# Optimization experiments

Hardware: AMD Instinct MI355X
Metric: run time of the kernel (lower is better)

Reference implementation:

```python
import jax, jax.numpy as jnp
import numpy as np

N_NODES = 50000
N_EDGES = 800000
HIDDEN = 64
NUM_FEATURES = 1
OUT_DIM = 2


def setup_inputs() -> dict:
    key = jax.random.key(0)
    k = jax.random.split(key, 6)
    x = jax.random.normal(k[0], (N_NODES, NUM_FEATURES), dtype=jnp.float32)
    edge_index = jax.random.randint(k[1], (2, N_EDGES), 0, N_NODES, dtype=jnp.int32)
    # GCNConv params (PyG default: glorot weight, zero bias; random here for testing)
    W1 = jax.random.normal(k[2], (NUM_FEATURES, HIDDEN), dtype=jnp.float32) * 0.5
    b1 = jax.random.normal(k[3], (HIDDEN,), dtype=jnp.float32) * 0.1
    W2 = jax.random.normal(k[4], (HIDDEN, OUT_DIM), dtype=jnp.float32) * 0.1
    b2 = jax.random.normal(k[5], (OUT_DIM,), dtype=jnp.float32) * 0.1
    return {"x": x, "edge_index": edge_index, "W1": W1, "b1": b1, "W2": W2, "b2": b2}


def _gcn_norm(edge_index, num_nodes):
    # PyG gcn_norm with add_self_loops=True, symmetric normalization
    row, col = edge_index[0], edge_index[1]
    loop = jnp.arange(num_nodes, dtype=row.dtype)
    row = jnp.concatenate([row, loop])
    col = jnp.concatenate([col, loop])
    ew = jnp.ones(row.shape[0], dtype=jnp.float32)
    deg = jax.ops.segment_sum(ew, col, num_segments=num_nodes)  # in-degree incl. self-loop
    dinv = jnp.where(deg > 0, jax.lax.rsqrt(deg), 0.0)
    norm = dinv[row] * dinv[col]  # [E+N]
    return row, col, norm


def _gcn_conv(x, row, col, norm, W, b, num_nodes):
    h = x @ W                                  # [N, out] transform first (out <= in here is fine)
    msg = h[row] * norm[:, None]               # gather + scale, [E+N, out]
    out = jax.ops.segment_sum(msg, col, num_segments=num_nodes)  # scatter-add at targets
    return out + b


def reference(x, edge_index, W1, b1, W2, b2):
    row, col, norm = _gcn_norm(edge_index, N_NODES)
    h = _gcn_conv(x, row, col, norm, W1, b1, N_NODES)
    h = jax.nn.relu(h)
    out = _gcn_conv(h, row, col, norm, W2, b2, N_NODES)
    return out
```

## Files before the change

kernel.cpp:

```cpp
#include <hip/hip_runtime.h>
#include <math.h>

#define N_NODES 50000
#define N_EDGES 800000
#define HIDDEN  64
#define MAXDEG  64
#define NPB     64
#define NCHUNK  256
#define CHUNK   (N_EDGES / NCHUNK)
#define NGROUP  (N_NODES / 4)


__global__ __launch_bounds__(256)
void k_hist(const int* __restrict__ col, unsigned* __restrict__ part) {
    __shared__ unsigned h[NGROUP];
    const int c = blockIdx.x;
    for (int i = threadIdx.x; i < NGROUP; i += 256) h[i] = 0u;
    __syncthreads();
    const int* cc = col + c * CHUNK;
    for (int i = threadIdx.x; i < CHUNK; i += 256) {
        int n = cc[i];
        atomicAdd(&h[n >> 2], 1u << ((n & 3) * 8));
    }
    __syncthreads();
    unsigned* dst = part + (size_t)c * NGROUP;
    for (int i = threadIdx.x; i < NGROUP; i += 256) dst[i] = h[i];
}

__global__ __launch_bounds__(256)
void k_scan(unsigned* __restrict__ part, const float* __restrict__ x,
            unsigned* __restrict__ cntPacked, float* __restrict__ g) {
    int i = blockIdx.x * 256 + threadIdx.x;
    if (i >= NGROUP) return;
    unsigned run = 0;
    for (int c0 = 0; c0 < NCHUNK; c0 += 8) {
        unsigned v[8];
#pragma unroll
        for (int k = 0; k < 8; ++k) v[k] = part[(size_t)(c0 + k) * NGROUP + i];
#pragma unroll
        for (int k = 0; k < 8; ++k) {
            part[(size_t)(c0 + k) * NGROUP + i] = run;
            run += v[k];
        }
    }
    cntPacked[i] = run;
    int n0 = i * 4;
#pragma unroll
    for (int b = 0; b < 4; ++b) {
        int deg = (int)((run >> (8 * b)) & 255u);
        int n = n0 + b;
        g[n] = rsqrtf((float)(min(deg, MAXDEG) + 1)) * x[n];
    }
}

__global__ __launch_bounds__(256)
void k_place(const int* __restrict__ row, const int* __restrict__ col,
             const unsigned char* __restrict__ baseBytes,
             unsigned short* __restrict__ ell) {
    __shared__ unsigned h[NGROUP];
    const int c = blockIdx.x;
    for (int i = threadIdx.x; i < NGROUP; i += 256) h[i] = 0u;
    __syncthreads();
    const int* cc = col + c * CHUNK;
    const int* rr = row + c * CHUNK;
    const unsigned char* gb = baseBytes + (size_t)c * (size_t)N_NODES;
    for (int i = threadIdx.x; i < CHUNK; i += 256) {
        int n = cc[i];
        int sh = (n & 3) * 8;
        unsigned old = atomicAdd(&h[n >> 2], 1u << sh);
        int j = (int)((old >> sh) & 255u) + (int)gb[n];
        if (j < MAXDEG) ell[(size_t)j * N_NODES + n] = (unsigned short)rr[i];
    }
}

__global__ __launch_bounds__(512)
void k_layer1(const unsigned short* __restrict__ ell, const unsigned* __restrict__ cntPacked,
              const float* __restrict__ g,
              const float* __restrict__ W1, const float* __restrict__ b1,
              const float* __restrict__ W2, float2* __restrict__ z) {
    __shared__ float red[8][NPB];
    const int w = threadIdx.x >> 6;
    const int l = threadIdx.x & 63;
    const int n = blockIdx.x * NPB + l;
    const bool valid = (n < N_NODES);
    int d = valid ? min((int)((cntPacked[n >> 2] >> ((n & 3) * 8)) & 255u), MAXDEG) : 0;
    float acc = 0.0f;
    for (int j = w; j < d; j += 8)
        acc += g[ell[(size_t)j * N_NODES + n]];
    red[w][l] = acc;
    __syncthreads();
    if (w == 0 && valid) {
        float a = red[0][l] + red[1][l] + red[2][l] + red[3][l]
                + red[4][l] + red[5][l] + red[6][l] + red[7][l];
        float di = rsqrtf((float)(d + 1));
        float sv = di * (a + g[n]);
        float y0 = 0.0f, y1 = 0.0f;
#pragma unroll
        for (int k = 0; k < HIDDEN; ++k) {
            float h = fmaxf(sv * W1[k] + b1[k], 0.0f);
            y0 += h * W2[2 * k];
            y1 += h * W2[2 * k + 1];
        }
        z[n] = make_float2(di * y0, di * y1);
    }
}

__global__ __launch_bounds__(512)
void k_layer2(const unsigned short* __restrict__ ell, const unsigned* __restrict__ cntPacked,
              const float2* __restrict__ z, const float* __restrict__ b2,
              float2* __restrict__ out) {
    __shared__ float2 red[8][NPB];
    const int w = threadIdx.x >> 6;
    const int l = threadIdx.x & 63;
    const int n = blockIdx.x * NPB + l;
    const bool valid = (n < N_NODES);
    int d = valid ? min((int)((cntPacked[n >> 2] >> ((n & 3) * 8)) & 255u), MAXDEG) : 0;
    float T0 = 0.0f, T1 = 0.0f;
    for (int j = w; j < d; j += 8) {
        float2 v = z[ell[(size_t)j * N_NODES + n]];
        T0 += v.x; T1 += v.y;
    }
    red[w][l] = make_float2(T0, T1);
    __syncthreads();
    if (w == 0 && valid) {
        float Tx = 0.0f, Ty = 0.0f;
#pragma unroll
        for (int k = 0; k < 8; ++k) { Tx += red[k][l].x; Ty += red[k][l].y; }
        float di = rsqrtf((float)(d + 1));
        float2 zn = z[n];
        out[n] = make_float2(di * (Tx + zn.x) + b2[0], di * (Ty + zn.y) + b2[1]);
    }
}


extern "C" void kernel_launch(void* const* d_in, const int* in_sizes, int n_in,
                              void* d_out, int out_size, void* d_ws, size_t ws_size,
                              hipStream_t stream) {
    const float* x  = (const float*)d_in[0];
    const int*   ei = (const int*)d_in[1];
    const float* W1 = (const float*)d_in[2];
    const float* b1 = (const float*)d_in[3];
    const float* W2 = (const float*)d_in[4];
    const float* b2 = (const float*)d_in[5];

    const int* row = ei;
    const int* col = ei + N_EDGES;

    unsigned* part      = (unsigned*)d_ws;
    unsigned* cntPacked = part + (size_t)NCHUNK * NGROUP;
    float*    g         = (float*)(cntPacked + NGROUP);
    float2*   z         = (float2*)(g + N_NODES);
    unsigned short* ell = (unsigned short*)(z + N_NODES);

    const int gS = (NGROUP + 255) / 256;
    const int gL = (N_NODES + NPB - 1) / NPB;

    k_hist  <<<NCHUNK, 256, 0, stream>>>(col, part);
    k_scan  <<<gS, 256, 0, stream>>>(part, x, cntPacked, g);
    k_place <<<NCHUNK, 256, 0, stream>>>(row, col, (const unsigned char*)part, ell);
    k_layer1<<<gL, 512, 0, stream>>>(ell, cntPacked, g, W1, b1, W2, z);
    k_layer2<<<gL, 512, 0, stream>>>(ell, cntPacked, z, b2, (float2*)d_out);
}
```

Baseline: 121.1 us.

## Replace ELL build with LDS-privatized scatter-add aggregation per node range

Drops the exclusive scan and the ELL placement kernel. Each layer's aggregation now scatters edge contributions into shared-memory float accumulators covering a node-range slice, writes per-chunk partial sums, and a follow-up kernel reduces them. The MAXDEG cap goes away, so the degree handling is exact. The cost is that every block rereads the full edge chunk for each node slice, large partial-sum buffers are written and reduced, and the shared-memory float atomics may contend.

```diff
diff --git a/kernel.cpp b/kernel.cpp
--- a/kernel.cpp
+++ b/kernel.cpp
@@ -4,11 +4,15 @@
 #define N_NODES 50000
 #define N_EDGES 800000
 #define HIDDEN  64
-#define MAXDEG  64
-#define NPB     64
-#define NCHUNK  256
-#define CHUNK   (N_EDGES / NCHUNK)
-#define NGROUP  (N_NODES / 4)
+#define NGROUP  12500
+#define NHC     256
+#define HCHUNK  (N_EDGES / NHC)
+#define HALF    25000
+#define NC1     125
+#define C1      (N_EDGES / NC1)
+#define QTR     12500
+#define NC2     64
+#define C2      (N_EDGES / NC2)
 
 
 __global__ __launch_bounds__(256)
@@ -17,8 +21,8 @@
     const int c = blockIdx.x;
     for (int i = threadIdx.x; i < NGROUP; i += 256) h[i] = 0u;
     __syncthreads();
-    const int* cc = col + c * CHUNK;
-    for (int i = threadIdx.x; i < CHUNK; i += 256) {
+    const int* cc = col + c * HCHUNK;
+    for (int i = threadIdx.x; i < HCHUNK; i += 256) {
         int n = cc[i];
         atomicAdd(&h[n >> 2], 1u << ((n & 3) * 8));
     }
@@ -28,108 +32,126 @@
 }
 
 __global__ __launch_bounds__(256)
-void k_scan(unsigned* __restrict__ part, const float* __restrict__ x,
-            unsigned* __restrict__ cntPacked, float* __restrict__ g) {
+void k_g(const unsigned* __restrict__ part, const float* __restrict__ x,
+         float* __restrict__ dinv, float* __restrict__ g) {
     int i = blockIdx.x * 256 + threadIdx.x;
     if (i >= NGROUP) return;
-    unsigned run = 0;
-    for (int c0 = 0; c0 < NCHUNK; c0 += 8) {
+    unsigned sum = 0;
+    for (int c0 = 0; c0 < NHC; c0 += 8) {
         unsigned v[8];
 #pragma unroll
         for (int k = 0; k < 8; ++k) v[k] = part[(size_t)(c0 + k) * NGROUP + i];
 #pragma unroll
-        for (int k = 0; k < 8; ++k) {
-            part[(size_t)(c0 + k) * NGROUP + i] = run;
-            run += v[k];
-        }
+        for (int k = 0; k < 8; ++k) sum += v[k];
     }
-    cntPacked[i] = run;
     int n0 = i * 4;
 #pragma unroll
     for (int b = 0; b < 4; ++b) {
-        int deg = (int)((run >> (8 * b)) & 255u);
-        int n = n0 + b;
-        g[n] = rsqrtf((float)(min(deg, MAXDEG) + 1)) * x[n];
-    }
-}
-
-__global__ __launch_bounds__(256)
-void k_place(const int* __restrict__ row, const int* __restrict__ col,
-             const unsigned char* __restrict__ baseBytes,
-             unsigned short* __restrict__ ell) {
-    __shared__ unsigned h[NGROUP];
-    const int c = blockIdx.x;
-    for (int i = threadIdx.x; i < NGROUP; i += 256) h[i] = 0u;
-    __syncthreads();
-    const int* cc = col + c * CHUNK;
-    const int* rr = row + c * CHUNK;
-    const unsigned char* gb = baseBytes + (size_t)c * (size_t)N_NODES;
-    for (int i = threadIdx.x; i < CHUNK; i += 256) {
-        int n = cc[i];
-        int sh = (n & 3) * 8;
-        unsigned old = atomicAdd(&h[n >> 2], 1u << sh);
-        int j = (int)((old >> sh) & 255u) + (int)gb[n];
-        if (j < MAXDEG) ell[(size_t)j * N_NODES + n] = (unsigned short)rr[i];
+        int deg = (int)((sum >> (8 * b)) & 255u);
+        float di = rsqrtf((float)(deg + 1));
+        dinv[n0 + b] = di;
+        g[n0 + b] = di * x[n0 + b];
     }
 }
 
 __global__ __launch_bounds__(512)
-void k_layer1(const unsigned short* __restrict__ ell, const unsigned* __restrict__ cntPacked,
-              const float* __restrict__ g,
-              const float* __restrict__ W1, const float* __restrict__ b1,
-              const float* __restrict__ W2, float2* __restrict__ z) {
-    __shared__ float red[8][NPB];
-    const int w = threadIdx.x >> 6;
-    const int l = threadIdx.x & 63;
-    const int n = blockIdx.x * NPB + l;
-    const bool valid = (n < N_NODES);
-    int d = valid ? min((int)((cntPacked[n >> 2] >> ((n & 3) * 8)) & 255u), MAXDEG) : 0;
-    float acc = 0.0f;
-    for (int j = w; j < d; j += 8)
-        acc += g[ell[(size_t)j * N_NODES + n]];
-    red[w][l] = acc;
+void k_agg1(const int* __restrict__ row, const int* __restrict__ col,
+            const float* __restrict__ g, float* __restrict__ part1) {
+    __shared__ float acc[HALF];
+    const int half = blockIdx.x / NC1;
+    const int ch   = blockIdx.x % NC1;
+    const int lo   = half * HALF;
+    for (int i = threadIdx.x; i < HALF; i += 512) acc[i] = 0.0f;
     __syncthreads();
-    if (w == 0 && valid) {
-        float a = red[0][l] + red[1][l] + red[2][l] + red[3][l]
-                + red[4][l] + red[5][l] + red[6][l] + red[7][l];
-        float di = rsqrtf((float)(d + 1));
-        float sv = di * (a + g[n]);
-        float y0 = 0.0f, y1 = 0.0f;
+    const int e0 = ch * C1;
+    const int4* c4 = (const int4*)(col + e0);
+    const int4* r4 = (const int4*)(row + e0);
+    for (int i = threadIdx.x; i < C1 / 4; i += 512) {
+        int4 cv = c4[i];
+        int4 rv = r4[i];
+        unsigned a;
+        a = (unsigned)(cv.x - lo); if (a < HALF) atomicAdd(&acc[a], g[rv.x]);
+        a = (unsigned)(cv.y - lo); if (a < HALF) atomicAdd(&acc[a], g[rv.y]);
+        a = (unsigned)(cv.z - lo); if (a < HALF) atomicAdd(&acc[a], g[rv.z]);
+        a = (unsigned)(cv.w - lo); if (a < HALF) atomicAdd(&acc[a], g[rv.w]);
+    }
+    __syncthreads();
+    float* dst = part1 + (size_t)blockIdx.x * HALF;
+    for (int i = threadIdx.x; i < HALF; i += 512) dst[i] = acc[i];
+}
+
+__global__ __launch_bounds__(256)
+void k_mlp(const float* __restrict__ part1, const float* __restrict__ g,
+           const float* __restrict__ dinv,
+           const float* __restrict__ W1, const float* __restrict__ b1,
+           const float* __restrict__ W2, float2* __restrict__ z) {
+    int n = blockIdx.x * 256 + threadIdx.x;
+    if (n >= N_NODES) return;
+    int h = n / HALF, nl = n % HALF;
+    const float* p = part1 + (size_t)h * NC1 * HALF + nl;
+    float t = 0.0f;
+#pragma unroll 5
+    for (int c = 0; c < NC1; ++c) t += p[(size_t)c * HALF];
+    float di = dinv[n];
+    float sv = di * (t + g[n]);
+    float y0 = 0.0f, y1 = 0.0f;
 #pragma unroll
-        for (int k = 0; k < HIDDEN; ++k) {
-            float h = fmaxf(sv * W1[k] + b1[k], 0.0f);
-            y0 += h * W2[2 * k];
-            y1 += h * W2[2 * k + 1];
-        }
-        z[n] = make_float2(di * y0, di * y1);
+    for (int k = 0; k < HIDDEN; ++k) {
+        float hh = fmaxf(sv * W1[k] + b1[k], 0.0f);
+        y0 += hh * W2[2 * k];
+        y1 += hh * W2[2 * k + 1];
     }
+    z[n] = make_float2(di * y0, di * y1);
 }
 
 __global__ __launch_bounds__(512)
-void k_layer2(const unsigned short* __restrict__ ell, const unsigned* __restrict__ cntPacked,
-              const float2* __restrict__ z, const float* __restrict__ b2,
-              float2* __restrict__ out) {
-    __shared__ float2 red[8][NPB];
-    const int w = threadIdx.x >> 6;
-    const int l = threadIdx.x & 63;
-    const int n = blockIdx.x * NPB + l;
-    const bool valid = (n < N_NODES);
-    int d = valid ? min((int)((cntPacked[n >> 2] >> ((n & 3) * 8)) & 255u), MAXDEG) : 0;
-    float T0 = 0.0f, T1 = 0.0f;
-    for (int j = w; j < d; j += 8) {
-        float2 v = z[ell[(size_t)j * N_NODES + n]];
-        T0 += v.x; T1 += v.y;
+void k_agg2(const int* __restrict__ row, const int* __restrict__ col,
+            const float2* __restrict__ z, float2* __restrict__ part2) {
+    __shared__ float ax[QTR];
+    __shared__ float ay[QTR];
+    const int q  = blockIdx.x >> 6;
+    const int ch = blockIdx.x & 63;
+    const int lo = q * QTR;
+    for (int i = threadIdx.x; i < QTR; i += 512) { ax[i] = 0.0f; ay[i] = 0.0f; }
+    __syncthreads();
+    const int e0 = ch * C2;
+    const int4* c4 = (const int4*)(col + e0);
+    const int4* r4 = (const int4*)(row + e0);
+    for (int i = threadIdx.x; i < C2 / 4; i += 512) {
+        int4 cv = c4[i];
+        int4 rv = r4[i];
+        unsigned a;
+        a = (unsigned)(cv.x - lo);
+        if (a < QTR) { float2 v = z[rv.x]; atomicAdd(&ax[a], v.x); atomicAdd(&ay[a], v.y); }
+        a = (unsigned)(cv.y - lo);
+        if (a < QTR) { float2 v = z[rv.y]; atomicAdd(&ax[a], v.x); atomicAdd(&ay[a], v.y); }
+        a = (unsigned)(cv.z - lo);
+        if (a < QTR) { float2 v = z[rv.z]; atomicAdd(&ax[a], v.x); atomicAdd(&ay[a], v.y); }
+        a = (unsigned)(cv.w - lo);
+        if (a < QTR) { float2 v = z[rv.w]; atomicAdd(&ax[a], v.x); atomicAdd(&ay[a], v.y); }
     }
-    red[w][l] = make_float2(T0, T1);
     __syncthreads();
-    if (w == 0 && valid) {
-        float Tx = 0.0f, Ty = 0.0f;
-#pragma unroll
-        for (int k = 0; k < 8; ++k) { Tx += red[k][l].x; Ty += red[k][l].y; }
-        float di = rsqrtf((float)(d + 1));
-        float2 zn = z[n];
-        out[n] = make_float2(di * (Tx + zn.x) + b2[0], di * (Ty + zn.y) + b2[1]);
+    float2* dst = part2 + (size_t)blockIdx.x * QTR;
+    for (int i = threadIdx.x; i < QTR; i += 512) dst[i] = make_float2(ax[i], ay[i]);
+}
+
+__global__ __launch_bounds__(256)
+void k_final(const float2* __restrict__ part2, const float2* __restrict__ z,
+             const float* __restrict__ dinv, const float* __restrict__ b2,
+             float2* __restrict__ out) {
+    int n = blockIdx.x * 256 + threadIdx.x;
+    if (n >= N_NODES) return;
+    int q = n / QTR, nl = n % QTR;
+    const float2* p = part2 + (size_t)q * NC2 * QTR + nl;
+    float Tx = 0.0f, Ty = 0.0f;
+#pragma unroll 8
+    for (int c = 0; c < NC2; ++c) {
+        float2 v = p[(size_t)c * QTR];
+        Tx += v.x; Ty += v.y;
     }
+    float di = dinv[n];
+    float2 zn = z[n];
+    out[n] = make_float2(di * (Tx + zn.x) + b2[0], di * (Ty + zn.y) + b2[1]);
 }
 
 
@@ -146,18 +168,21 @@
     const int* row = ei;
     const int* col = ei + N_EDGES;
 
-    unsigned* part      = (unsigned*)d_ws;
-    unsigned* cntPacked = part + (size_t)NCHUNK * NGROUP;
-    float*    g         = (float*)(cntPacked + NGROUP);
-    float2*   z         = (float2*)(g + N_NODES);
-    unsigned short* ell = (unsigned short*)(z + N_NODES);
+    char* p = (char*)d_ws;
+    unsigned* histPart = (unsigned*)p;  p += (size_t)NHC * NGROUP * 4;
+    float*    part1    = (float*)p;     p += (size_t)2 * NC1 * HALF * 4;
+    float2*   part2    = (float2*)p;    p += (size_t)4 * NC2 * QTR * 8;
+    float*    dinv     = (float*)p;     p += N_NODES * 4;
+    float*    g        = (float*)p;     p += N_NODES * 4;
+    float2*   z        = (float2*)p;
 
-    const int gS = (NGROUP + 255) / 256;
-    const int gL = (N_NODES + NPB - 1) / NPB;
+    const int gG = (NGROUP + 255) / 256;
+    const int gN = (N_NODES + 255) / 256;
 
-    k_hist  <<<NCHUNK, 256, 0, stream>>>(col, part);
-    k_scan  <<<gS, 256, 0, stream>>>(part, x, cntPacked, g);
-    k_place <<<NCHUNK, 256, 0, stream>>>(row, col, (const unsigned char*)part, ell);
-    k_layer1<<<gL, 512, 0, stream>>>(ell, cntPacked, g, W1, b1, W2, z);
-    k_layer2<<<gL, 512, 0, stream>>>(ell, cntPacked, z, b2, (float2*)d_out);
+    k_hist <<<NHC,       256, 0, stream>>>(col, histPart);
+    k_g    <<<gG,        256, 0, stream>>>(histPart, x, dinv, g);
+    k_agg1 <<<2 * NC1,   512, 0, stream>>>(row, col, g, part1);
+    k_mlp  <<<gN,        256, 0, stream>>>(part1, g, dinv, W1, b1, W2, z);
+    k_agg2 <<<4 * NC2,   512, 0, stream>>>(row, col, z, part2);
+    k_final<<<gN,        256, 0, stream>>>(part2, z, dinv, b2, (float2*)d_out);
 }
```

Measured after the change: 136.7 us. +12.9%, slower.
